# Performance work log

Hardware: AMD Instinct MI355X
Metric: run time of the kernel (lower is better)

Reference implementation:

```python
import jax, jax.numpy as jnp
import numpy as np

N_NODES = 50000
N_EDGES = 800000
IN_DIM = 256
H1 = 512
H2 = 128


def _gcn_conv(x, W, b, row, col, ew, n_nodes):
    """PyG GCNConv with edge_weight: linear (no bias) -> add self-loops ->
    symmetric normalization -> weighted scatter-add -> + bias."""
    xw = x @ W  # [N, out]
    loop = jnp.arange(n_nodes, dtype=row.dtype)
    row_f = jnp.concatenate([row, loop])
    col_f = jnp.concatenate([col, loop])
    ew_f = jnp.concatenate([ew, jnp.ones((n_nodes,), dtype=ew.dtype)])
    deg = jax.ops.segment_sum(ew_f, col_f, num_segments=n_nodes)  # in-degree
    dinv = jnp.where(deg > 0, jax.lax.rsqrt(jnp.where(deg > 0, deg, 1.0)), 0.0)
    norm = dinv[row_f] * ew_f * dinv[col_f]  # [E+N]
    msg = norm[:, None] * xw[row_f]          # [E+N, out] gather
    out = jax.ops.segment_sum(msg, col_f, num_segments=n_nodes)  # scatter-add
    return out + b


def _prelu(x, alpha):
    return jnp.where(x >= 0, x, alpha * x)


def setup_inputs() -> dict:
    key = jax.random.key(0)
    ks = jax.random.split(key, 6)
    x = jax.random.normal(ks[0], (N_NODES, IN_DIM), dtype=jnp.float32)
    edge_index = jax.random.randint(ks[1], (2, N_EDGES), 0, N_NODES, dtype=jnp.int32)
    edge_attr = jax.random.uniform(ks[2], (N_EDGES,), dtype=jnp.float32)
    W1 = jax.random.normal(ks[3], (IN_DIM, H1), dtype=jnp.float32) / np.sqrt(IN_DIM)
    b1 = jnp.zeros((H1,), dtype=jnp.float32)
    W2 = jax.random.normal(ks[4], (H1, H2), dtype=jnp.float32) / np.sqrt(H1)
    b2 = jnp.zeros((H2,), dtype=jnp.float32)
    alpha = jnp.ones((1,), dtype=jnp.float32) * 0.25  # nn.PReLU default init
    return {"x": x, "edge_attr": edge_attr, "W1": W1, "b1": b1,
            "W2": W2, "b2": b2, "alpha": alpha, "edge_index": edge_index}


def reference(x, edge_attr, W1, b1, W2, b2, alpha, edge_index):
    row, col = edge_index[0], edge_index[1]
    # Dropout treated as identity (deterministic eval-mode reference).
    feat1 = _prelu(_gcn_conv(x, W1, b1, row, col, edge_attr, N_NODES), alpha)
    feat2 = _prelu(_gcn_conv(feat1, W2, b2, row, col, edge_attr, N_NODES), alpha)
    return feat2
```

## Files before the change

kernel.cpp:

```cpp
#include <hip/hip_runtime.h>

#define N_NODES 50000
#define N_EDGES 800000
#define IN_DIM  256
#define H1      512
#define H2      128

typedef __attribute__((ext_vector_type(8))) short  short8v;
typedef __attribute__((ext_vector_type(4))) float  float4v;
typedef __attribute__((ext_vector_type(4))) unsigned uint4v;

__device__ __forceinline__ void split_bf16(float v, unsigned short& h, unsigned short& l) {
    unsigned u = __builtin_bit_cast(unsigned, v);
    unsigned hr = (u + 0x7FFFu + ((u >> 16) & 1u)) >> 16;
    float hf = __builtin_bit_cast(float, hr << 16);
    float lf = v - hf;
    unsigned ul = __builtin_bit_cast(unsigned, lf);
    unsigned lr = (ul + 0x7FFFu + ((ul >> 16) & 1u)) >> 16;
    h = (unsigned short)hr; l = (unsigned short)lr;
}


__global__ void init_kernel(float* deg, int* cnt, int n) {
    int i = blockIdx.x * blockDim.x + threadIdx.x;
    if (i < n) { deg[i] = 1.0f; cnt[i] = 0; }
}

__global__ void edge_deg_kernel(const int* __restrict__ col, const float* __restrict__ ew,
                                float* deg, int* cnt, int ne) {
    int e = blockIdx.x * blockDim.x + threadIdx.x;
    if (e < ne) {
        int c = col[e];
        atomicAdd(&deg[c], ew[e]);
        atomicAdd(&cnt[c], 1);
    }
}

__global__ void dinv_kernel(const float* __restrict__ deg, float* dinv, int n) {
    int i = blockIdx.x * blockDim.x + threadIdx.x;
    if (i < n) dinv[i] = rsqrtf(deg[i]);
}

__global__ void scan_block_kernel(const int* __restrict__ cnt, int* __restrict__ part,
                                  int* __restrict__ bsum, int n) {
    __shared__ int s[256];
    int tid = threadIdx.x;
    int i = blockIdx.x * 256 + tid;
    int v = (i < n) ? cnt[i] : 0;
    s[tid] = v; __syncthreads();
#pragma unroll
    for (int d = 1; d < 256; d <<= 1) {
        int t = (tid >= d) ? s[tid - d] : 0; __syncthreads();
        s[tid] += t; __syncthreads();
    }
    if (i < n) part[i] = s[tid] - v;
    if (tid == 255) bsum[blockIdx.x] = s[255];
}

__global__ void scan_tops_kernel(const int* __restrict__ bsum, int* __restrict__ boff, int nb) {
    __shared__ int s[256];
    int tid = threadIdx.x;
    int v = (tid < nb) ? bsum[tid] : 0;
    s[tid] = v; __syncthreads();
#pragma unroll
    for (int d = 1; d < 256; d <<= 1) {
        int t = (tid >= d) ? s[tid - d] : 0; __syncthreads();
        s[tid] += t; __syncthreads();
    }
    if (tid < nb) boff[tid] = s[tid] - v;
}

__global__ void scan_add_kernel(const int* __restrict__ part, const int* __restrict__ boff,
                                int* __restrict__ ptr, int* __restrict__ fill, int n) {
    int i = blockIdx.x * 256 + threadIdx.x;
    if (i < n) {
        int p = part[i] + boff[blockIdx.x];
        ptr[i] = p; fill[i] = p;
    }
    if (i == 0) ptr[n] = N_EDGES;
}

__global__ void scatter_kernel(const int* __restrict__ row, const int* __restrict__ col,
                               const float* __restrict__ ew, const float* __restrict__ dinv,
                               int* fill, int2* __restrict__ edges, int ne) {
    int e = blockIdx.x * blockDim.x + threadIdx.x;
    if (e < ne) {
        int r = row[e], c = col[e];
        int pos = atomicAdd(&fill[c], 1);
        float w = dinv[r] * ew[e] * dinv[c];
        edges[pos] = make_int2(r, __float_as_int(w));
    }
}

__global__ void convw_kernel(const float* __restrict__ W, unsigned short* __restrict__ Wh,
                             unsigned short* __restrict__ Wl, int K, int N) {
    int idx = blockIdx.x * 256 + threadIdx.x;
    if (idx < N * K) {
        int n = idx / K, k = idx % K;
        unsigned short h, l;
        split_bf16(W[(size_t)k * N + n], h, l);
        Wh[idx] = h; Wl[idx] = l;
    }
}


__global__ __launch_bounds__(256) void agg256_half_kernel(
        const float* __restrict__ x, const float* __restrict__ dinv,
        const int* __restrict__ ptr, const int2* __restrict__ edges,
        unsigned short* __restrict__ out_h, unsigned short* __restrict__ out_l, int d0) {
    int wv = threadIdx.x >> 6, lane = threadIdx.x & 63;
    int node = blockIdx.x * 4 + wv;
    if (node >= N_NODES) return;
    const float* xb = x + d0 + lane * 2;
    float di = dinv[node];
    float s = di * di;
    float2 v = *(const float2*)(xb + (size_t)node * IN_DIM);
    float ax = v.x * s, ay = v.y * s;
    int j = ptr[node], e1 = ptr[node + 1];
    for (; j + 3 < e1; j += 4) {
        int2 e0 = edges[j], e1_ = edges[j + 1], e2 = edges[j + 2], e3 = edges[j + 3];
        float2 u0 = *(const float2*)(xb + (size_t)e0.x * IN_DIM);
        float2 u1 = *(const float2*)(xb + (size_t)e1_.x * IN_DIM);
        float2 u2 = *(const float2*)(xb + (size_t)e2.x * IN_DIM);
        float2 u3 = *(const float2*)(xb + (size_t)e3.x * IN_DIM);
        float c0 = __int_as_float(e0.y), c1 = __int_as_float(e1_.y);
        float c2 = __int_as_float(e2.y), c3 = __int_as_float(e3.y);
        ax += c0 * u0.x + c1 * u1.x + c2 * u2.x + c3 * u3.x;
        ay += c0 * u0.y + c1 * u1.y + c2 * u2.y + c3 * u3.y;
    }
    for (; j < e1; ++j) {
        int2 e0 = edges[j];
        float c0 = __int_as_float(e0.y);
        float2 u0 = *(const float2*)(xb + (size_t)e0.x * IN_DIM);
        ax += c0 * u0.x; ay += c0 * u0.y;
    }
    unsigned short h0, l0, h1, l1;
    split_bf16(ax, h0, l0);
    split_bf16(ay, h1, l1);
    size_t o = (size_t)node * IN_DIM + d0;
    ((unsigned*)(out_h + o))[lane] = (unsigned)h0 | ((unsigned)h1 << 16);
    ((unsigned*)(out_l + o))[lane] = (unsigned)l0 | ((unsigned)l1 << 16);
}

__global__ __launch_bounds__(256) void agg128_epi_kernel(
        const float* __restrict__ xw, const float* __restrict__ dinv,
        const int* __restrict__ ptr, const int2* __restrict__ edges,
        const float* __restrict__ b2, const float* __restrict__ alphap,
        float* __restrict__ out) {
    int wv = threadIdx.x >> 6, lane = threadIdx.x & 63;
    int node = blockIdx.x * 4 + wv;
    if (node >= N_NODES) return;
    const float2* x2 = (const float2*)xw;
    float di = dinv[node];
    float s = di * di;
    float2 v = x2[node * 64 + lane];
    float ax = v.x * s, ay = v.y * s;
    int j = ptr[node], e1 = ptr[node + 1];
    for (; j + 3 < e1; j += 4) {
        int2 e0 = edges[j], e1_ = edges[j + 1], e2 = edges[j + 2], e3 = edges[j + 3];
        float2 u0 = x2[e0.x * 64 + lane];
        float2 u1 = x2[e1_.x * 64 + lane];
        float2 u2 = x2[e2.x * 64 + lane];
        float2 u3 = x2[e3.x * 64 + lane];
        float c0 = __int_as_float(e0.y), c1 = __int_as_float(e1_.y);
        float c2 = __int_as_float(e2.y), c3 = __int_as_float(e3.y);
        ax += c0 * u0.x + c1 * u1.x + c2 * u2.x + c3 * u3.x;
        ay += c0 * u0.y + c1 * u1.y + c2 * u2.y + c3 * u3.y;
    }
    for (; j < e1; ++j) {
        int2 e0 = edges[j];
        float c0 = __int_as_float(e0.y);
        float2 u0 = x2[e0.x * 64 + lane];
        ax += c0 * u0.x; ay += c0 * u0.y;
    }
    float alpha = alphap[0];
    float2 b = ((const float2*)b2)[lane];
    ax += b.x; ay += b.y;
    ax = (ax >= 0.f) ? ax : alpha * ax;
    ay = (ay >= 0.f) ? ay : alpha * ay;
    ((float2*)out)[node * 64 + lane] = make_float2(ax, ay);
}


__device__ __forceinline__ int swz(int row, int k ) {
    return ((row << 7) + (k << 1)) ^ ((row & 7) << 4);
}

__device__ __forceinline__ void gload16(const void* g, void* l) {
    __builtin_amdgcn_global_load_lds(
        (const __attribute__((address_space(1))) unsigned int*)g,
        (__attribute__((address_space(3))) unsigned int*)l, 16, 0, 0);
}

__device__ __forceinline__ void stage_plane_async(
        const unsigned short* __restrict__ gbase,
        unsigned short* lds, int K, int grow0, int k0, int wave, int lane) {
    int r8 = lane >> 3;
    int kk = k0 + (((lane & 7) ^ r8) << 3);
#pragma unroll
    for (int t = 0; t < 4; ++t) {
        int rowblk = wave * 32 + t * 8;
        const unsigned short* g = gbase + (size_t)(grow0 + rowblk + r8) * K + kk;
        gload16(g, lds + (size_t)rowblk * 64);
    }
}

template <int MODE>
__global__ __launch_bounds__(256, 2) void gemm_mfma_kernel(
        const unsigned short* __restrict__ A_hi, const unsigned short* __restrict__ A_lo,
        const unsigned short* __restrict__ B_hi, const unsigned short* __restrict__ B_lo,
        const float* __restrict__ bias, const float* __restrict__ alphap,
        unsigned short* __restrict__ Oh, unsigned short* __restrict__ Ol,
        float* __restrict__ Of, int M, int N, int K, int tilesX) {
    __shared__ unsigned short smem[4][8192];
    unsigned short* Ah = smem[0];
    unsigned short* Al = smem[1];
    unsigned short* Bh = smem[2];
    unsigned short* Bl = smem[3];

    const int tid  = threadIdx.x;
    const int lane = tid & 63, wave = tid >> 6;
    const int wm = wave >> 1, wn = wave & 1;
    const int lr = lane & 15, lk = (lane >> 4) << 3;

    const int nwg = gridDim.x;
    const int q_ = nwg >> 3, r_ = nwg & 7;
    const int xcd = blockIdx.x & 7, idx = blockIdx.x >> 3;
    const int wg = ((xcd < r_) ? xcd * (q_ + 1) : r_ * (q_ + 1) + (xcd - r_) * q_) + idx;
    const int m0 = (wg / tilesX) * 128, n0 = (wg % tilesX) * 128;

    float4v acc[4][4] = {};

    stage_plane_async(A_hi, Ah, K, m0, 0, wave, lane);
    stage_plane_async(A_lo, Al, K, m0, 0, wave, lane);
    stage_plane_async(B_hi, Bh, K, n0, 0, wave, lane);
    stage_plane_async(B_lo, Bl, K, n0, 0, wave, lane);

    for (int k0 = 0; k0 < K; k0 += 64) {
        __syncthreads();
        short8v ah[2][4], al[2][4], bh[2][4], bl[2][4];
#pragma unroll
        for (int q = 0; q < 2; ++q)
#pragma unroll
            for (int i = 0; i < 4; ++i) {
                ah[q][i] = *(const short8v*)((const char*)Ah + swz(wm * 64 + i * 16 + lr, q * 32 + lk));
                al[q][i] = *(const short8v*)((const char*)Al + swz(wm * 64 + i * 16 + lr, q * 32 + lk));
                bh[q][i] = *(const short8v*)((const char*)Bh + swz(wn * 64 + i * 16 + lr, q * 32 + lk));
                bl[q][i] = *(const short8v*)((const char*)Bl + swz(wn * 64 + i * 16 + lr, q * 32 + lk));
            }
        __syncthreads();
        if (k0 + 64 < K) {
            stage_plane_async(A_hi, Ah, K, m0, k0 + 64, wave, lane);
            stage_plane_async(A_lo, Al, K, m0, k0 + 64, wave, lane);
            stage_plane_async(B_hi, Bh, K, n0, k0 + 64, wave, lane);
            stage_plane_async(B_lo, Bl, K, n0, k0 + 64, wave, lane);
        }
#pragma unroll
        for (int q = 0; q < 2; ++q)
#pragma unroll
            for (int mi = 0; mi < 4; ++mi)
#pragma unroll
                for (int ni = 0; ni < 4; ++ni) {
                    acc[mi][ni] = __builtin_amdgcn_mfma_f32_16x16x32_bf16(ah[q][mi], bh[q][ni], acc[mi][ni], 0, 0, 0);
                    acc[mi][ni] = __builtin_amdgcn_mfma_f32_16x16x32_bf16(ah[q][mi], bl[q][ni], acc[mi][ni], 0, 0, 0);
                    acc[mi][ni] = __builtin_amdgcn_mfma_f32_16x16x32_bf16(al[q][mi], bh[q][ni], acc[mi][ni], 0, 0, 0);
                }
    }

    if (MODE == 1) {
        unsigned* tr = (unsigned*)smem;
        const float alpha = alphap[0];
#pragma unroll
        for (int mi = 0; mi < 4; ++mi)
#pragma unroll
            for (int ni = 0; ni < 4; ++ni) {
                int lcol = wn * 64 + ni * 16 + lr;
                float bv = bias[n0 + lcol];
#pragma unroll
                for (int r = 0; r < 4; ++r) {
                    int lrow = wm * 64 + mi * 16 + (lane >> 4) * 4 + r;
                    float v = acc[mi][ni][r] + bv;
                    v = (v >= 0.f) ? v : alpha * v;
                    unsigned short h, l;
                    split_bf16(v, h, l);
                    tr[lrow * 128 + lcol] = (unsigned)h | ((unsigned)l << 16);
                }
            }
        __syncthreads();
#pragma unroll
        for (int c = 0; c < 8; ++c) {
            int chunk = tid + c * 256;
            int row = chunk >> 4, cb = (chunk & 15) * 8;
            int grow = m0 + row;
            if (grow < M) {
                const unsigned* p = tr + row * 128 + cb;
                uint4v u0 = *(const uint4v*)p;
                uint4v u1 = *(const uint4v*)(p + 4);
                short8v hv, lv;
#pragma unroll
                for (int i = 0; i < 4; ++i) {
                    hv[i]     = (short)(u0[i] & 0xFFFFu); lv[i]     = (short)(u0[i] >> 16);
                    hv[i + 4] = (short)(u1[i] & 0xFFFFu); lv[i + 4] = (short)(u1[i] >> 16);
                }
                *(short8v*)(Oh + (size_t)grow * N + n0 + cb) = hv;
                *(short8v*)(Ol + (size_t)grow * N + n0 + cb) = lv;
            }
        }
    } else {
        float* tr = (float*)smem;
#pragma unroll
        for (int mi = 0; mi < 4; ++mi)
#pragma unroll
            for (int ni = 0; ni < 4; ++ni) {
                int lcol = wn * 64 + ni * 16 + lr;
#pragma unroll
                for (int r = 0; r < 4; ++r) {
                    int lrow = wm * 64 + mi * 16 + (lane >> 4) * 4 + r;
                    tr[lrow * 128 + lcol] = acc[mi][ni][r];
                }
            }
        __syncthreads();
#pragma unroll
        for (int c = 0; c < 8; ++c) {
            int chunk = tid + c * 256;
            int row = chunk >> 4, cb = (chunk & 15) * 8;
            int grow = m0 + row;
            if (grow < M) {
                const float* p = tr + row * 128 + cb;
                float4 a = *(const float4*)p;
                float4 b = *(const float4*)(p + 4);
                *(float4*)(Of + (size_t)grow * N + n0 + cb)     = a;
                *(float4*)(Of + (size_t)grow * N + n0 + cb + 4) = b;
            }
        }
    }
}


extern "C" void kernel_launch(void* const* d_in, const int* in_sizes, int n_in,
                              void* d_out, int out_size, void* d_ws, size_t ws_size,
                              hipStream_t stream) {
    const float* x     = (const float*)d_in[0];
    const float* eattr = (const float*)d_in[1];
    const float* W1    = (const float*)d_in[2];
    const float* b1    = (const float*)d_in[3];
    const float* W2    = (const float*)d_in[4];
    const float* b2    = (const float*)d_in[5];
    const float* alpha = (const float*)d_in[6];
    const int*   eidx  = (const int*)d_in[7];
    const int* row = eidx;
    const int* col = eidx + N_EDGES;
    float* out = (float*)d_out;

    float* ws_f = (float*)d_ws;
    size_t off = 0;
    float* deg   = ws_f + off; off += N_NODES;
    float* dinv  = ws_f + off; off += N_NODES;
    int2*  edges = (int2*)(ws_f + off); off += (size_t)2 * N_EDGES;
    unsigned short* aggx_h = (unsigned short*)(ws_f + off); off += (size_t)N_NODES * IN_DIM / 2;
    unsigned short* aggx_l = (unsigned short*)(ws_f + off); off += (size_t)N_NODES * IN_DIM / 2;
    float* xw2 = (float*)aggx_h;
    unsigned short* feat1_h = (unsigned short*)(ws_f + off); off += (size_t)N_NODES * H1 / 2;
    unsigned short* feat1_l = (unsigned short*)(ws_f + off); off += (size_t)N_NODES * H1 / 2;
    unsigned short* W1t_h = (unsigned short*)(ws_f + off); off += (size_t)IN_DIM * H1 / 2;
    unsigned short* W1t_l = (unsigned short*)(ws_f + off); off += (size_t)IN_DIM * H1 / 2;
    unsigned short* W2t_h = (unsigned short*)(ws_f + off); off += (size_t)H1 * H2 / 2;
    unsigned short* W2t_l = (unsigned short*)(ws_f + off); off += (size_t)H1 * H2 / 2;
    int* cnt  = (int*)(ws_f + off); off += N_NODES;
    int* ptr  = (int*)(ws_f + off); off += N_NODES + 1;
    int* fill = (int*)(ws_f + off); off += N_NODES;
    int* part = (int*)(ws_f + off); off += N_NODES;
    int* bsum = (int*)(ws_f + off); off += 256;
    int* boff = (int*)(ws_f + off); off += 256;

    const int nodeBlocks = (N_NODES + 255) / 256;
    const int edgeBlocks = (N_EDGES + 255) / 256;

    convw_kernel<<<(IN_DIM * H1 + 255) / 256, 256, 0, stream>>>(W1, W1t_h, W1t_l, IN_DIM, H1);
    convw_kernel<<<(H1 * H2 + 255) / 256, 256, 0, stream>>>(W2, W2t_h, W2t_l, H1, H2);

    init_kernel<<<nodeBlocks, 256, 0, stream>>>(deg, cnt, N_NODES);
    edge_deg_kernel<<<edgeBlocks, 256, 0, stream>>>(col, eattr, deg, cnt, N_EDGES);
    dinv_kernel<<<nodeBlocks, 256, 0, stream>>>(deg, dinv, N_NODES);
    scan_block_kernel<<<nodeBlocks, 256, 0, stream>>>(cnt, part, bsum, N_NODES);
    scan_tops_kernel<<<1, 256, 0, stream>>>(bsum, boff, nodeBlocks);
    scan_add_kernel<<<nodeBlocks, 256, 0, stream>>>(part, boff, ptr, fill, N_NODES);
    scatter_kernel<<<edgeBlocks, 256, 0, stream>>>(row, col, eattr, dinv, fill, edges, N_EDGES);

    agg256_half_kernel<<<(N_NODES + 3) / 4, 256, 0, stream>>>(x, dinv, ptr, edges, aggx_h, aggx_l, 0);
    agg256_half_kernel<<<(N_NODES + 3) / 4, 256, 0, stream>>>(x, dinv, ptr, edges, aggx_h, aggx_l, 128);
    {
        int tilesX = H1 / 128, tilesY = (N_NODES + 127) / 128;
        gemm_mfma_kernel<1><<<tilesX * tilesY, 256, 0, stream>>>(
            aggx_h, aggx_l, W1t_h, W1t_l, b1, alpha, feat1_h, feat1_l, nullptr,
            N_NODES, H1, IN_DIM, tilesX);
    }

    {
        int tilesX = H2 / 128, tilesY = (N_NODES + 127) / 128;
        gemm_mfma_kernel<0><<<tilesX * tilesY, 256, 0, stream>>>(
            feat1_h, feat1_l, W2t_h, W2t_l, nullptr, nullptr, nullptr, nullptr, xw2,
            N_NODES, H2, H1, tilesX);
    }
    agg128_epi_kernel<<<(N_NODES + 3) / 4, 256, 0, stream>>>(xw2, dinv, ptr, edges, b2, alpha, out);
}
```

Baseline: 488.3 us.

## Compute degrees from CSR segments instead of float atomics

Drops the float atomicAdd degree accumulation and instead sums edge weights per destination segment after the CSR scatter, followed by a separate pass that rewrites each edge weight into its normalized coefficient. This removes 800k float atomics and two small kernels. In exchange it adds two per-node sequential loops over the CSR with uncoalesced, thread-per-node access and an extra read-modify-write of the edge array. The float summation order also changes, which slightly alters rounding but makes it deterministic.

```diff
diff --git a/kernel.cpp b/kernel.cpp
--- a/kernel.cpp
+++ b/kernel.cpp
@@ -21,24 +21,9 @@
 }
 
 
-__global__ void init_kernel(float* deg, int* cnt, int n) {
-    int i = blockIdx.x * blockDim.x + threadIdx.x;
-    if (i < n) { deg[i] = 1.0f; cnt[i] = 0; }
-}
-
-__global__ void edge_deg_kernel(const int* __restrict__ col, const float* __restrict__ ew,
-                                float* deg, int* cnt, int ne) {
+__global__ void edge_hist_kernel(const int* __restrict__ col, int* cnt, int ne) {
     int e = blockIdx.x * blockDim.x + threadIdx.x;
-    if (e < ne) {
-        int c = col[e];
-        atomicAdd(&deg[c], ew[e]);
-        atomicAdd(&cnt[c], 1);
-    }
-}
-
-__global__ void dinv_kernel(const float* __restrict__ deg, float* dinv, int n) {
-    int i = blockIdx.x * blockDim.x + threadIdx.x;
-    if (i < n) dinv[i] = rsqrtf(deg[i]);
+    if (e < ne) atomicAdd(&cnt[col[e]], 1);
 }
 
 __global__ void scan_block_kernel(const int* __restrict__ cnt, int* __restrict__ part,
@@ -81,14 +66,38 @@
 }
 
 __global__ void scatter_kernel(const int* __restrict__ row, const int* __restrict__ col,
-                               const float* __restrict__ ew, const float* __restrict__ dinv,
+                               const float* __restrict__ ew,
                                int* fill, int2* __restrict__ edges, int ne) {
     int e = blockIdx.x * blockDim.x + threadIdx.x;
     if (e < ne) {
         int r = row[e], c = col[e];
         int pos = atomicAdd(&fill[c], 1);
-        float w = dinv[r] * ew[e] * dinv[c];
-        edges[pos] = make_int2(r, __float_as_int(w));
+        edges[pos] = make_int2(r, __float_as_int(ew[e]));
+    }
+}
+
+__global__ void degdinv_kernel(const int* __restrict__ ptr, const int2* __restrict__ edges,
+                               float* __restrict__ dinv, int n) {
+    int i = blockIdx.x * blockDim.x + threadIdx.x;
+    if (i < n) {
+        float s = 1.0f;
+        int e1 = ptr[i + 1];
+        for (int j = ptr[i]; j < e1; ++j) s += __int_as_float(edges[j].y);
+        dinv[i] = rsqrtf(s);
+    }
+}
+
+__global__ void coef_kernel(const int* __restrict__ ptr, int2* __restrict__ edges,
+                            const float* __restrict__ dinv, int n) {
+    int i = blockIdx.x * blockDim.x + threadIdx.x;
+    if (i < n) {
+        float dc = dinv[i];
+        int e1 = ptr[i + 1];
+        for (int j = ptr[i]; j < e1; ++j) {
+            int2 t = edges[j];
+            float w = __int_as_float(t.y);
+            edges[j] = make_int2(t.x, __float_as_int(dinv[t.x] * w * dc));
+        }
     }
 }
 
@@ -354,7 +363,6 @@
 
     float* ws_f = (float*)d_ws;
     size_t off = 0;
-    float* deg   = ws_f + off; off += N_NODES;
     float* dinv  = ws_f + off; off += N_NODES;
     int2*  edges = (int2*)(ws_f + off); off += (size_t)2 * N_EDGES;
     unsigned short* aggx_h = (unsigned short*)(ws_f + off); off += (size_t)N_NODES * IN_DIM / 2;
@@ -379,13 +387,14 @@
     convw_kernel<<<(IN_DIM * H1 + 255) / 256, 256, 0, stream>>>(W1, W1t_h, W1t_l, IN_DIM, H1);
     convw_kernel<<<(H1 * H2 + 255) / 256, 256, 0, stream>>>(W2, W2t_h, W2t_l, H1, H2);
 
-    init_kernel<<<nodeBlocks, 256, 0, stream>>>(deg, cnt, N_NODES);
-    edge_deg_kernel<<<edgeBlocks, 256, 0, stream>>>(col, eattr, deg, cnt, N_EDGES);
-    dinv_kernel<<<nodeBlocks, 256, 0, stream>>>(deg, dinv, N_NODES);
+    hipMemsetAsync(cnt, 0, N_NODES * sizeof(int), stream);
+    edge_hist_kernel<<<edgeBlocks, 256, 0, stream>>>(col, cnt, N_EDGES);
     scan_block_kernel<<<nodeBlocks, 256, 0, stream>>>(cnt, part, bsum, N_NODES);
     scan_tops_kernel<<<1, 256, 0, stream>>>(bsum, boff, nodeBlocks);
     scan_add_kernel<<<nodeBlocks, 256, 0, stream>>>(part, boff, ptr, fill, N_NODES);
-    scatter_kernel<<<edgeBlocks, 256, 0, stream>>>(row, col, eattr, dinv, fill, edges, N_EDGES);
+    scatter_kernel<<<edgeBlocks, 256, 0, stream>>>(row, col, eattr, fill, edges, N_EDGES);
+    degdinv_kernel<<<nodeBlocks, 256, 0, stream>>>(ptr, edges, dinv, N_NODES);
+    coef_kernel<<<nodeBlocks, 256, 0, stream>>>(ptr, edges, dinv, N_NODES);
 
     agg256_half_kernel<<<(N_NODES + 3) / 4, 256, 0, stream>>>(x, dinv, ptr, edges, aggx_h, aggx_l, 0);
     agg256_half_kernel<<<(N_NODES + 3) / 4, 256, 0, stream>>>(x, dinv, ptr, edges, aggx_h, aggx_l, 128);
```

Measured after the change: 495.7 us. About the same (+1.5%).
